# Performance work log

Hardware: AMD Instinct MI355X
Metric: run time of the kernel (lower is better)

Reference implementation:

```python
import jax, jax.numpy as jnp
import numpy as np

EMBED_DIM = 256
NUM_HEADS = 4
HEAD_DIM = EMBED_DIM // NUM_HEADS
SCALE = HEAD_DIM ** (-0.5)


def setup_inputs() -> dict:
    key = jax.random.key(0)
    kx, kq, kp, kb = jax.random.split(key, 4)
    B, N, C = 4, 4096, EMBED_DIM
    x = jax.random.normal(kx, (B, N, C), dtype=jnp.float32)
    # qkv: Linear(C, 3C, bias=False); torch stores weight as [out, in]
    w_qkv = jax.random.normal(kq, (3 * C, C), dtype=jnp.float32) * (C ** -0.5)
    w_proj = jax.random.normal(kp, (C, C), dtype=jnp.float32) * (C ** -0.5)
    b_proj = jax.random.normal(kb, (C,), dtype=jnp.float32) * 0.01
    return {"x": x, "w_qkv": w_qkv, "w_proj": w_proj, "b_proj": b_proj}


def reference(x, w_qkv, w_proj, b_proj):
    B, N, C = x.shape
    H, D = NUM_HEADS, HEAD_DIM
    # qkv projection: [B,N,3C] -> [3,B,H,N,D]
    qkv = (x @ w_qkv.T).reshape(B, N, 3, H, D).transpose(2, 0, 3, 1, 4)
    q, k, v = qkv[0], qkv[1], qkv[2]
    # materialized [B,H,N,N] scores (faithful to the original)
    attn = jnp.einsum("bhnd,bhmd->bhnm", q, k) * SCALE
    attn_probs = jax.nn.softmax(attn, axis=-1)
    out = jnp.einsum("bhnm,bhmd->bhnd", attn_probs, v)
    out = out.transpose(0, 2, 1, 3).reshape(B, N, C)
    return out @ w_proj.T + b_proj
```

## Files before the change

kernel.cpp:

```cpp
#include <hip/hip_runtime.h>
#include <hip/hip_bf16.h>

typedef __hip_bfloat16 bf16;
typedef _Float16 f16;
typedef __attribute__((ext_vector_type(8))) short bf16x8;
typedef __attribute__((ext_vector_type(8))) _Float16 f16x8;
typedef __attribute__((ext_vector_type(2))) _Float16 f16x2;
typedef __attribute__((ext_vector_type(4))) float f32x4;
typedef __attribute__((ext_vector_type(4))) unsigned int u32x4;
typedef __attribute__((ext_vector_type(2))) unsigned int u32x2;

#define B_ 4
#define N_ 4096
#define C_ 256
#define H_ 4
#define D_ 64
#define KLN 0.18033688011112042f

#if __has_builtin(__builtin_amdgcn_exp2f)
#define EXP2(x) __builtin_amdgcn_exp2f(x)
#else
#define EXP2(x) exp2f(x)
#endif
#if __has_builtin(__builtin_amdgcn_rcpf)
#define RCP(x) __builtin_amdgcn_rcpf(x)
#else
#define RCP(x) (1.0f / (x))
#endif

__device__ inline void load_lds16(const void* g, void* l) {
#if __has_builtin(__builtin_amdgcn_global_load_lds)
    __builtin_amdgcn_global_load_lds(
        (const __attribute__((address_space(1))) unsigned int*)g,
        (__attribute__((address_space(3))) unsigned int*)l, 16, 0, 0);
#else
    int ln = __lane_id();
    ((u32x4*)l)[ln] = *((const u32x4*)g);
#endif
}

__device__ inline unsigned int pk2(float a, float b) {
    unsigned int ua = __builtin_bit_cast(unsigned int, a) + 0x8000u;
    unsigned int ub = __builtin_bit_cast(unsigned int, b) + 0x8000u;
    return (ua >> 16) | (ub & 0xffff0000u);
}
__device__ inline unsigned int pkh2(float a, float b) {
#if __has_builtin(__builtin_amdgcn_cvt_pkrtz)
    return __builtin_bit_cast(unsigned int, __builtin_amdgcn_cvt_pkrtz(a, b));
#else
    f16x2 h = { (f16)a, (f16)b };
    return __builtin_bit_cast(unsigned int, h);
#endif
}
__device__ inline short f2s(float x) {
    return (short)__builtin_bit_cast(unsigned short, __float2bfloat16(x));
}
__device__ inline bf16x8 cvt8(const float* __restrict__ p) {
    f32x4 a = *reinterpret_cast<const f32x4*>(p);
    f32x4 b = *reinterpret_cast<const f32x4*>(p + 4);
    bf16x8 r = { f2s(a[0]), f2s(a[1]), f2s(a[2]), f2s(a[3]),
                 f2s(b[0]), f2s(b[1]), f2s(b[2]), f2s(b[3]) };
    return r;
}

__global__ __launch_bounds__(256) void cast_bf16(const float* __restrict__ x,
                                                 const float* __restrict__ wq,
                                                 const float* __restrict__ wp,
                                                 bf16* __restrict__ xb,
                                                 bf16* __restrict__ wqb,
                                                 bf16* __restrict__ wpb)
{
    int bid = blockIdx.x;
    const float* s; bf16* d; int base;
    if (bid < 2048)      { s = x;  d = xb;  base = bid * 2048; }
    else if (bid < 2144) { s = wq; d = wqb; base = (bid - 2048) * 2048; }
    else                 { s = wp; d = wpb; base = (bid - 2144) * 2048; }
    int i = base + threadIdx.x * 8;
    f32x4 a = *reinterpret_cast<const f32x4*>(s + i);
    f32x4 b = *reinterpret_cast<const f32x4*>(s + i + 4);
    u32x4 o;
    o.x = pk2(a[0], a[1]); o.y = pk2(a[2], a[3]);
    o.z = pk2(b[0], b[1]); o.w = pk2(b[2], b[3]);
    *reinterpret_cast<u32x4*>(d + i) = o;
}

__global__ __launch_bounds__(256, 2) void qkv_fast(const bf16* __restrict__ x,
                                                   const bf16* __restrict__ w,
                                                   bf16* __restrict__ qw,
                                                   bf16* __restrict__ kw,
                                                   f16* __restrict__ vtw)
{
    __shared__ short w_s[64][264];
    const int tid  = threadIdx.x;
    const int lane = tid & 63;
    const int wav  = tid >> 6;
    const int quad = lane >> 4;
    const int l16  = lane & 15;
    const int mt = blockIdx.x / 12, nb = blockIdx.x % 12;
    const int m0 = mt * 64, n0 = nb * 64;

    {
        const int row = tid >> 2, cb = (tid & 3) * 64;
        const bf16* src = w + (size_t)(n0 + row) * C_ + cb;
#pragma unroll
        for (int i = 0; i < 8; ++i)
            *reinterpret_cast<bf16x8*>(&w_s[row][cb + i * 8]) =
                *reinterpret_cast<const bf16x8*>(src + i * 8);
    }
    __syncthreads();

    f32x4 acc[4] = {{0,0,0,0},{0,0,0,0},{0,0,0,0},{0,0,0,0}};
    const bf16* xrow = x + (size_t)(m0 + wav * 16 + l16) * C_ + quad * 8;
#pragma unroll
    for (int k0 = 0; k0 < C_; k0 += 32) {
        bf16x8 a = *reinterpret_cast<const bf16x8*>(xrow + k0);
#pragma unroll
        for (int nt = 0; nt < 4; ++nt) {
            bf16x8 b = *reinterpret_cast<const bf16x8*>(&w_s[nt * 16 + l16][k0 + quad * 8]);
            acc[nt] = __builtin_amdgcn_mfma_f32_16x16x32_bf16(a, b, acc[nt], 0, 0, 0);
        }
    }

    const int bb = m0 >> 12;
    const int nbase = (m0 + wav * 16) & (N_ - 1);
    if (nb < 4) {
        const int h = nb;
#pragma unroll
        for (int nt = 0; nt < 4; ++nt)
#pragma unroll
            for (int r = 0; r < 4; ++r) {
                int n = nbase + quad * 4 + r, d = nt * 16 + l16;
                qw[(((size_t)bb * H_ + h) * N_ + n) * D_ + d] =
                    __float2bfloat16(acc[nt][r] * KLN);
            }
    } else if (nb < 8) {
        const int h = nb - 4;
#pragma unroll
        for (int nt = 0; nt < 4; ++nt)
#pragma unroll
            for (int r = 0; r < 4; ++r) {
                int n = nbase + quad * 4 + r, d = nt * 16 + l16;
                kw[(((size_t)bb * H_ + h) * N_ + n) * D_ + d] =
                    __float2bfloat16(acc[nt][r]);
            }
    } else {
        const int h = nb - 8;
#pragma unroll
        for (int nt = 0; nt < 4; ++nt) {
            int d = nt * 16 + l16;
            u32x2 wv;
            wv.x = pkh2(acc[nt][0], acc[nt][1]);
            wv.y = pkh2(acc[nt][2], acc[nt][3]);
            *reinterpret_cast<u32x2*>(
                vtw + (((size_t)bb * H_ + h) * D_ + d) * N_ + nbase + quad * 4) = wv;
        }
    }
}

__global__ __launch_bounds__(256) void qkv_cvt(const float* __restrict__ x,
                                               const float* __restrict__ w,
                                               bf16* __restrict__ qw,
                                               bf16* __restrict__ kw,
                                               f16* __restrict__ vtw)
{
    const int lane = threadIdx.x & 63;
    const int wav  = threadIdx.x >> 6;
    const int quad = lane >> 4;
    const int l16  = lane & 15;
    const int gw   = blockIdx.x * 4 + wav;
    const int m0   = (gw / 12) * 16;
    const int n0   = (gw % 12) * 64;

    f32x4 acc[4] = {{0,0,0,0},{0,0,0,0},{0,0,0,0},{0,0,0,0}};
    const float* xrow = x + (size_t)(m0 + l16) * C_ + quad * 8;
#pragma unroll
    for (int k0 = 0; k0 < C_; k0 += 32) {
        bf16x8 a = cvt8(xrow + k0);
#pragma unroll
        for (int nt = 0; nt < 4; ++nt) {
            bf16x8 b = cvt8(w + (size_t)(n0 + nt * 16 + l16) * C_ + k0 + quad * 8);
            acc[nt] = __builtin_amdgcn_mfma_f32_16x16x32_bf16(a, b, acc[nt], 0, 0, 0);
        }
    }
#pragma unroll
    for (int nt = 0; nt < 4; ++nt)
#pragma unroll
        for (int r = 0; r < 4; ++r) {
            int m  = m0 + quad * 4 + r;
            int o  = n0 + nt * 16 + l16;
            int bb = m >> 12;
            int n  = m & (N_ - 1);
            if (o < 256) {
                int h = o >> 6, d = o & 63;
                qw[(((size_t)bb * H_ + h) * N_ + n) * D_ + d] =
                    __float2bfloat16(acc[nt][r] * KLN);
            } else if (o < 512) {
                int oo = o - 256; int h = oo >> 6, d = oo & 63;
                kw[(((size_t)bb * H_ + h) * N_ + n) * D_ + d] =
                    __float2bfloat16(acc[nt][r]);
            } else {
                int oo = o - 512; int h = oo >> 6, d = oo & 63;
                vtw[(((size_t)bb * H_ + h) * D_ + d) * N_ + n] = (f16)acc[nt][r];
            }
        }
}

__global__ __launch_bounds__(256, 2) void attn(const bf16* __restrict__ q,
                                               const bf16* __restrict__ k,
                                               const f16* __restrict__ vt,
                                               bf16* __restrict__ o)
{
    __shared__ short        k_s[2][64 * 64];
    __shared__ f16          v_s[2][64 * 64];
    __shared__ unsigned int p_s[4][64 * 36];

    const int tid  = threadIdx.x;
    const int lane = tid & 63;
    const int wav  = tid >> 6;
    const int quad = lane >> 4;
    const int l16  = lane & 15;
    const int l8   = l16 & 7;
    const int sub  = wav & 1;
    const int jh   = wav >> 1;
    const int bh = blockIdx.x >> 5;
    const int qt = blockIdx.x & 31;
    const int bb = bh >> 2, h = bh & 3;

    const bf16* qp = q  + (size_t)bh * N_ * D_;
    const bf16* kp = k  + (size_t)bh * N_ * D_;
    const f16*  vp = vt + (size_t)bh * D_ * N_;

    const int qbase = qt * 128 + sub * 64;
    bf16x8 qb[4][2];
#pragma unroll
    for (int qg = 0; qg < 4; ++qg)
#pragma unroll
        for (int ks = 0; ks < 2; ++ks)
            qb[qg][ks] = *reinterpret_cast<const bf16x8*>(
                qp + (size_t)(qbase + qg * 16 + l16) * D_ + ks * 32 + quad * 8);

    const int ri = lane >> 3;
    const int ci = lane & 7;
    const int gc = ci ^ ri;

    f32x4 oacc[4][4];
    f32x4 lacc[4] = {{0,0,0,0},{0,0,0,0},{0,0,0,0},{0,0,0,0}};
#pragma unroll
    for (int qg = 0; qg < 4; ++qg)
#pragma unroll
        for (int dt = 0; dt < 4; ++dt) oacc[qg][dt] = (f32x4){0,0,0,0};
    const f16x8 onesA = {1.f16, 1.f16, 1.f16, 1.f16, 1.f16, 1.f16, 1.f16, 1.f16};

    for (int t = 0; t < 32; ++t) {
        const int j0 = jh * 2048 + t * 64;
        __syncthreads();
#pragma unroll
        for (int g = 0; g < 4; ++g) {
            const int rl_ = sub * 32 + g * 8;
            load_lds16(kp + (size_t)(j0 + rl_ + ri) * D_ + gc * 8, &k_s[jh][rl_ * 64]);
            load_lds16(vp + (size_t)(rl_ + ri) * N_ + j0 + gc * 8, &v_s[jh][rl_ * 64]);
        }
        __syncthreads();

        bf16x8 ka[4][2];
#pragma unroll
        for (int nt = 0; nt < 4; ++nt)
#pragma unroll
            for (int ks = 0; ks < 2; ++ks)
                ka[nt][ks] = *reinterpret_cast<const bf16x8*>(
                    &k_s[jh][(nt * 16 + l16) * 64 + (((ks << 2) + quad) ^ l8) * 8]);

#pragma unroll
        for (int qg = 0; qg < 4; ++qg) {
            f32x4 s[4] = {{0,0,0,0},{0,0,0,0},{0,0,0,0},{0,0,0,0}};
#pragma unroll
            for (int nt = 0; nt < 4; ++nt) {
                s[nt] = __builtin_amdgcn_mfma_f32_16x16x32_bf16(ka[nt][0], qb[qg][0], s[nt], 0, 0, 0);
                s[nt] = __builtin_amdgcn_mfma_f32_16x16x32_bf16(ka[nt][1], qb[qg][1], s[nt], 0, 0, 0);
            }
            unsigned int* prow = &p_s[wav][(qg * 16 + l16) * 36];
#pragma unroll
            for (int nt = 0; nt < 4; ++nt) {
                float p0 = EXP2(s[nt][0]);
                float p1 = EXP2(s[nt][1]);
                float p2 = EXP2(s[nt][2]);
                float p3 = EXP2(s[nt][3]);
                u32x2 w2 = { pkh2(p0, p1), pkh2(p2, p3) };
                *reinterpret_cast<u32x2*>(prow + nt * 8 + quad * 2) = w2;
            }
        }
        asm volatile("" ::: "memory");

#pragma unroll
        for (int ks = 0; ks < 2; ++ks) {
            f16x8 pb[4];
#pragma unroll
            for (int qg = 0; qg < 4; ++qg) {
                u32x4 pw = *reinterpret_cast<const u32x4*>(
                    &p_s[wav][(qg * 16 + l16) * 36 + ks * 16 + quad * 4]);
                pb[qg] = __builtin_bit_cast(f16x8, pw);
                lacc[qg] = __builtin_amdgcn_mfma_f32_16x16x32_f16(onesA, pb[qg], lacc[qg], 0, 0, 0);
            }
#pragma unroll
            for (int dt = 0; dt < 4; ++dt) {
                f16x8 va = *reinterpret_cast<const f16x8*>(
                    &v_s[jh][(dt * 16 + l16) * 64 + (((ks << 2) + quad) ^ l8) * 8]);
#pragma unroll
                for (int qg = 0; qg < 4; ++qg)
                    oacc[qg][dt] = __builtin_amdgcn_mfma_f32_16x16x32_f16(va, pb[qg], oacc[qg][dt], 0, 0, 0);
            }
        }
    }

    __syncthreads();
    float* mrg = reinterpret_cast<float*>(p_s);
    if (jh == 1) {
        float* dst = mrg + (sub * 64 + lane) * 68;
#pragma unroll
        for (int qg = 0; qg < 4; ++qg) {
#pragma unroll
            for (int dt = 0; dt < 4; ++dt)
#pragma unroll
                for (int e = 0; e < 4; ++e)
                    dst[qg * 17 + dt * 4 + e] = oacc[qg][dt][e];
            dst[qg * 17 + 16] = lacc[qg][0];
        }
    }
    __syncthreads();
    if (jh == 0) {
        const float* src = mrg + (sub * 64 + lane) * 68;
#pragma unroll
        for (int qg = 0; qg < 4; ++qg) {
            float rl = RCP(lacc[qg][0] + src[qg * 17 + 16]);
            const size_t obase = ((size_t)bb * N_ + qbase + qg * 16 + l16) * C_ + h * D_;
#pragma unroll
            for (int dt = 0; dt < 4; ++dt) {
                float v0 = (oacc[qg][dt][0] + src[qg * 17 + dt * 4 + 0]) * rl;
                float v1 = (oacc[qg][dt][1] + src[qg * 17 + dt * 4 + 1]) * rl;
                float v2 = (oacc[qg][dt][2] + src[qg * 17 + dt * 4 + 2]) * rl;
                float v3 = (oacc[qg][dt][3] + src[qg * 17 + dt * 4 + 3]) * rl;
                u32x2 wv = { pk2(v0, v1), pk2(v2, v3) };
                *reinterpret_cast<u32x2*>(o + obase + dt * 16 + quad * 4) = wv;
            }
        }
    }
}

__global__ __launch_bounds__(256, 2) void out_proj_fast(const bf16* __restrict__ ov,
                                                        const bf16* __restrict__ w,
                                                        const float* __restrict__ bias,
                                                        float* __restrict__ out)
{
    __shared__ short w_s[64][264];
    const int tid  = threadIdx.x;
    const int lane = tid & 63;
    const int wav  = tid >> 6;
    const int quad = lane >> 4;
    const int l16  = lane & 15;
    const int m0 = (blockIdx.x >> 2) * 64;
    const int n0 = (blockIdx.x & 3) * 64;

    {
        const int row = tid >> 2, cb = (tid & 3) * 64;
        const bf16* src = w + (size_t)(n0 + row) * C_ + cb;
#pragma unroll
        for (int i = 0; i < 8; ++i)
            *reinterpret_cast<bf16x8*>(&w_s[row][cb + i * 8]) =
                *reinterpret_cast<const bf16x8*>(src + i * 8);
    }
    __syncthreads();

    f32x4 acc[4] = {{0,0,0,0},{0,0,0,0},{0,0,0,0},{0,0,0,0}};
    const bf16* orow = ov + (size_t)(m0 + wav * 16 + l16) * C_ + quad * 8;
#pragma unroll
    for (int k0 = 0; k0 < C_; k0 += 32) {
        bf16x8 a = *reinterpret_cast<const bf16x8*>(orow + k0);
#pragma unroll
        for (int nt = 0; nt < 4; ++nt) {
            bf16x8 b = *reinterpret_cast<const bf16x8*>(&w_s[nt * 16 + l16][k0 + quad * 8]);
            acc[nt] = __builtin_amdgcn_mfma_f32_16x16x32_bf16(a, b, acc[nt], 0, 0, 0);
        }
    }
#pragma unroll
    for (int nt = 0; nt < 4; ++nt)
#pragma unroll
        for (int r = 0; r < 4; ++r) {
            int m  = m0 + wav * 16 + quad * 4 + r;
            int oc = n0 + nt * 16 + l16;
            out[(size_t)m * C_ + oc] = acc[nt][r] + bias[oc];
        }
}

__global__ __launch_bounds__(256) void out_proj_cvt(const bf16* __restrict__ ov,
                                                    const float* __restrict__ w,
                                                    const float* __restrict__ bias,
                                                    float* __restrict__ out)
{
    const int lane = threadIdx.x & 63;
    const int wav  = threadIdx.x >> 6;
    const int quad = lane >> 4;
    const int l16  = lane & 15;
    const int gw   = blockIdx.x * 4 + wav;
    const int m0   = (gw >> 2) * 16;
    const int n0   = (gw & 3) * 64;

    f32x4 acc[4] = {{0,0,0,0},{0,0,0,0},{0,0,0,0},{0,0,0,0}};
    const bf16* orow = ov + (size_t)(m0 + l16) * C_ + quad * 8;
#pragma unroll
    for (int k0 = 0; k0 < C_; k0 += 32) {
        bf16x8 a = *reinterpret_cast<const bf16x8*>(orow + k0);
#pragma unroll
        for (int nt = 0; nt < 4; ++nt) {
            bf16x8 b = cvt8(w + (size_t)(n0 + nt * 16 + l16) * C_ + k0 + quad * 8);
            acc[nt] = __builtin_amdgcn_mfma_f32_16x16x32_bf16(a, b, acc[nt], 0, 0, 0);
        }
    }
#pragma unroll
    for (int nt = 0; nt < 4; ++nt)
#pragma unroll
        for (int r = 0; r < 4; ++r) {
            int m  = m0 + quad * 4 + r;
            int oc = n0 + nt * 16 + l16;
            out[(size_t)m * C_ + oc] = acc[nt][r] + bias[oc];
        }
}

extern "C" void kernel_launch(void* const* d_in, const int* in_sizes, int n_in,
                              void* d_out, int out_size, void* d_ws, size_t ws_size,
                              hipStream_t stream) {
    const float* x      = (const float*)d_in[0];
    const float* w_qkv  = (const float*)d_in[1];
    const float* w_proj = (const float*)d_in[2];
    const float* b_proj = (const float*)d_in[3];
    float* out = (float*)d_out;

    const size_t qkv_elems = (size_t)B_ * H_ * N_ * D_;
    bf16* q_ws  = (bf16*)d_ws;
    bf16* k_ws  = q_ws  + qkv_elems;
    f16*  vt_ws = (f16*)(k_ws + qkv_elems);
    bf16* o_ws  = (bf16*)(vt_ws + qkv_elems);
    bf16* x_bf  = o_ws  + qkv_elems;
    bf16* wq_bf = x_bf  + (size_t)B_ * N_ * C_;
    bf16* wp_bf = wq_bf + (size_t)3 * C_ * C_;

    const size_t need = ((size_t)4 * qkv_elems + (size_t)B_ * N_ * C_
                         + (size_t)3 * C_ * C_ + (size_t)C_ * C_) * 2;

    if (ws_size >= need) {
        cast_bf16    <<<2176, 256, 0, stream>>>(x, w_qkv, w_proj, x_bf, wq_bf, wp_bf);
        qkv_fast     <<<3072, 256, 0, stream>>>(x_bf, wq_bf, q_ws, k_ws, vt_ws);
        attn         <<< 512, 256, 0, stream>>>(q_ws, k_ws, vt_ws, o_ws);
        out_proj_fast<<<1024, 256, 0, stream>>>(o_ws, wp_bf, b_proj, out);
    } else {
        qkv_cvt      <<<3072, 256, 0, stream>>>(x, w_qkv, q_ws, k_ws, vt_ws);
        attn         <<< 512, 256, 0, stream>>>(q_ws, k_ws, vt_ws, o_ws);
        out_proj_cvt <<<1024, 256, 0, stream>>>(o_ws, w_proj, b_proj, out);
    }
}
```

Baseline: 186.5 us.

## Fuse casts into projections and prepack K/V for LDS-free attention

Removes the separate bf16 cast kernel and converts fp32 x and weights inside the QKV and output projection kernels. The QKV kernel now writes K and V^T in a fragment-packed layout so the attention kernel loads MFMA operands straight from global memory into registers, with K double-buffered across tiles, instead of staging K/V through LDS behind barriers. The row-sum is now accumulated with scalar adds and cross-lane shuffles rather than an extra MFMA against a ones vector, and block indexing is remapped for locality. In exchange, attention depends on direct global loads with no LDS reuse across waves, which raises global and L2 traffic and register pressure.

Result: slower. 301.4 us (+61.6%).

```diff
diff --git a/kernel.cpp b/kernel.cpp
--- a/kernel.cpp
+++ b/kernel.cpp
@@ -28,17 +28,6 @@
 #define RCP(x) (1.0f / (x))
 #endif
 
-__device__ inline void load_lds16(const void* g, void* l) {
-#if __has_builtin(__builtin_amdgcn_global_load_lds)
-    __builtin_amdgcn_global_load_lds(
-        (const __attribute__((address_space(1))) unsigned int*)g,
-        (__attribute__((address_space(3))) unsigned int*)l, 16, 0, 0);
-#else
-    int ln = __lane_id();
-    ((u32x4*)l)[ln] = *((const u32x4*)g);
-#endif
-}
-
 __device__ inline unsigned int pk2(float a, float b) {
     unsigned int ua = __builtin_bit_cast(unsigned int, a) + 0x8000u;
     unsigned int ub = __builtin_bit_cast(unsigned int, b) + 0x8000u;
@@ -52,43 +41,18 @@
     return __builtin_bit_cast(unsigned int, h);
 #endif
 }
-__device__ inline short f2s(float x) {
-    return (short)__builtin_bit_cast(unsigned short, __float2bfloat16(x));
-}
 __device__ inline bf16x8 cvt8(const float* __restrict__ p) {
     f32x4 a = *reinterpret_cast<const f32x4*>(p);
     f32x4 b = *reinterpret_cast<const f32x4*>(p + 4);
-    bf16x8 r = { f2s(a[0]), f2s(a[1]), f2s(a[2]), f2s(a[3]),
-                 f2s(b[0]), f2s(b[1]), f2s(b[2]), f2s(b[3]) };
-    return r;
-}
-
-__global__ __launch_bounds__(256) void cast_bf16(const float* __restrict__ x,
-                                                 const float* __restrict__ wq,
-                                                 const float* __restrict__ wp,
-                                                 bf16* __restrict__ xb,
-                                                 bf16* __restrict__ wqb,
-                                                 bf16* __restrict__ wpb)
-{
-    int bid = blockIdx.x;
-    const float* s; bf16* d; int base;
-    if (bid < 2048)      { s = x;  d = xb;  base = bid * 2048; }
-    else if (bid < 2144) { s = wq; d = wqb; base = (bid - 2048) * 2048; }
-    else                 { s = wp; d = wpb; base = (bid - 2144) * 2048; }
-    int i = base + threadIdx.x * 8;
-    f32x4 a = *reinterpret_cast<const f32x4*>(s + i);
-    f32x4 b = *reinterpret_cast<const f32x4*>(s + i + 4);
-    u32x4 o;
-    o.x = pk2(a[0], a[1]); o.y = pk2(a[2], a[3]);
-    o.z = pk2(b[0], b[1]); o.w = pk2(b[2], b[3]);
-    *reinterpret_cast<u32x4*>(d + i) = o;
-}
-
-__global__ __launch_bounds__(256, 2) void qkv_fast(const bf16* __restrict__ x,
-                                                   const bf16* __restrict__ w,
-                                                   bf16* __restrict__ qw,
-                                                   bf16* __restrict__ kw,
-                                                   f16* __restrict__ vtw)
+    u32x4 r = { pk2(a[0], a[1]), pk2(a[2], a[3]), pk2(b[0], b[1]), pk2(b[2], b[3]) };
+    return __builtin_bit_cast(bf16x8, r);
+}
+
+__global__ __launch_bounds__(256, 2) void qkv_fused(const float* __restrict__ x,
+                                                    const float* __restrict__ w,
+                                                    bf16* __restrict__ qw,
+                                                    bf16* __restrict__ kw,
+                                                    f16* __restrict__ vtw)
 {
     __shared__ short w_s[64][264];
     const int tid  = threadIdx.x;
@@ -96,24 +60,28 @@
     const int wav  = tid >> 6;
     const int quad = lane >> 4;
     const int l16  = lane & 15;
-    const int mt = blockIdx.x / 12, nb = blockIdx.x % 12;
+    const int mt = blockIdx.x & 255, nb = blockIdx.x >> 8;
     const int m0 = mt * 64, n0 = nb * 64;
 
     {
         const int row = tid >> 2, cb = (tid & 3) * 64;
-        const bf16* src = w + (size_t)(n0 + row) * C_ + cb;
-#pragma unroll
-        for (int i = 0; i < 8; ++i)
-            *reinterpret_cast<bf16x8*>(&w_s[row][cb + i * 8]) =
-                *reinterpret_cast<const bf16x8*>(src + i * 8);
+        const float* src = w + (size_t)(n0 + row) * C_ + cb;
+#pragma unroll
+        for (int i = 0; i < 8; ++i) {
+            f32x4 a = *reinterpret_cast<const f32x4*>(src + i * 8);
+            f32x4 b = *reinterpret_cast<const f32x4*>(src + i * 8 + 4);
+            u32x4 pkd = { pk2(a[0], a[1]), pk2(a[2], a[3]),
+                          pk2(b[0], b[1]), pk2(b[2], b[3]) };
+            *reinterpret_cast<u32x4*>(&w_s[row][cb + i * 8]) = pkd;
+        }
     }
     __syncthreads();
 
     f32x4 acc[4] = {{0,0,0,0},{0,0,0,0},{0,0,0,0},{0,0,0,0}};
-    const bf16* xrow = x + (size_t)(m0 + wav * 16 + l16) * C_ + quad * 8;
+    const float* xrow = x + (size_t)(m0 + wav * 16 + l16) * C_ + quad * 8;
 #pragma unroll
     for (int k0 = 0; k0 < C_; k0 += 32) {
-        bf16x8 a = *reinterpret_cast<const bf16x8*>(xrow + k0);
+        bf16x8 a = cvt8(xrow + k0);
 #pragma unroll
         for (int nt = 0; nt < 4; ++nt) {
             bf16x8 b = *reinterpret_cast<const bf16x8*>(&w_s[nt * 16 + l16][k0 + quad * 8]);
@@ -135,83 +103,37 @@
             }
     } else if (nb < 8) {
         const int h = nb - 4;
-#pragma unroll
-        for (int nt = 0; nt < 4; ++nt)
-#pragma unroll
-            for (int r = 0; r < 4; ++r) {
-                int n = nbase + quad * 4 + r, d = nt * 16 + l16;
-                kw[(((size_t)bb * H_ + h) * N_ + n) * D_ + d] =
-                    __float2bfloat16(acc[nt][r]);
-            }
+        bf16* kb_ = kw + (size_t)(bb * H_ + h) * (N_ / 16) * 1024;
+        const int jblk = nbase >> 4;
+#pragma unroll
+        for (int nt = 0; nt < 4; ++nt) {
+            const int base = jblk * 1024 + (nt >> 1) * 512 +
+                             (((nt * 2) + (l16 >> 3)) & 3) * 128 + (l16 & 7);
+#pragma unroll
+            for (int r = 0; r < 4; ++r)
+                kb_[base + (quad * 4 + r) * 8] = __float2bfloat16(acc[nt][r]);
+        }
     } else {
         const int h = nb - 8;
+        f16* vb_ = vtw + (size_t)(bb * H_ + h) * (N_ / 64) * 4096;
+        const int jblk64 = nbase >> 6;
+        const int ksv    = (nbase >> 5) & 1;
+        const int quadv  = (((nbase & 31) + quad * 4) >> 3) & 3;
+        const int ev     = (quad & 1) * 4;
 #pragma unroll
         for (int nt = 0; nt < 4; ++nt) {
-            int d = nt * 16 + l16;
-            u32x2 wv;
-            wv.x = pkh2(acc[nt][0], acc[nt][1]);
-            wv.y = pkh2(acc[nt][2], acc[nt][3]);
+            u32x2 wv = { pkh2(acc[nt][0], acc[nt][1]), pkh2(acc[nt][2], acc[nt][3]) };
             *reinterpret_cast<u32x2*>(
-                vtw + (((size_t)bb * H_ + h) * D_ + d) * N_ + nbase + quad * 4) = wv;
-        }
-    }
-}
-
-__global__ __launch_bounds__(256) void qkv_cvt(const float* __restrict__ x,
-                                               const float* __restrict__ w,
-                                               bf16* __restrict__ qw,
-                                               bf16* __restrict__ kw,
-                                               f16* __restrict__ vtw)
-{
-    const int lane = threadIdx.x & 63;
-    const int wav  = threadIdx.x >> 6;
-    const int quad = lane >> 4;
-    const int l16  = lane & 15;
-    const int gw   = blockIdx.x * 4 + wav;
-    const int m0   = (gw / 12) * 16;
-    const int n0   = (gw % 12) * 64;
-
-    f32x4 acc[4] = {{0,0,0,0},{0,0,0,0},{0,0,0,0},{0,0,0,0}};
-    const float* xrow = x + (size_t)(m0 + l16) * C_ + quad * 8;
-#pragma unroll
-    for (int k0 = 0; k0 < C_; k0 += 32) {
-        bf16x8 a = cvt8(xrow + k0);
-#pragma unroll
-        for (int nt = 0; nt < 4; ++nt) {
-            bf16x8 b = cvt8(w + (size_t)(n0 + nt * 16 + l16) * C_ + k0 + quad * 8);
-            acc[nt] = __builtin_amdgcn_mfma_f32_16x16x32_bf16(a, b, acc[nt], 0, 0, 0);
-        }
-    }
-#pragma unroll
-    for (int nt = 0; nt < 4; ++nt)
-#pragma unroll
-        for (int r = 0; r < 4; ++r) {
-            int m  = m0 + quad * 4 + r;
-            int o  = n0 + nt * 16 + l16;
-            int bb = m >> 12;
-            int n  = m & (N_ - 1);
-            if (o < 256) {
-                int h = o >> 6, d = o & 63;
-                qw[(((size_t)bb * H_ + h) * N_ + n) * D_ + d] =
-                    __float2bfloat16(acc[nt][r] * KLN);
-            } else if (o < 512) {
-                int oo = o - 256; int h = oo >> 6, d = oo & 63;
-                kw[(((size_t)bb * H_ + h) * N_ + n) * D_ + d] =
-                    __float2bfloat16(acc[nt][r]);
-            } else {
-                int oo = o - 512; int h = oo >> 6, d = oo & 63;
-                vtw[(((size_t)bb * H_ + h) * D_ + d) * N_ + n] = (f16)acc[nt][r];
-            }
-        }
+                &vb_[jblk64 * 4096 + nt * 1024 + ksv * 512 + (quadv * 16 + l16) * 8 + ev]) = wv;
+        }
+    }
 }
 
 __global__ __launch_bounds__(256, 2) void attn(const bf16* __restrict__ q,
-                                               const bf16* __restrict__ k,
+                                               const bf16* __restrict__ kt,
                                                const f16* __restrict__ vt,
                                                bf16* __restrict__ o)
 {
-    __shared__ short        k_s[2][64 * 64];
-    __shared__ f16          v_s[2][64 * 64];
     __shared__ unsigned int p_s[4][64 * 36];
 
     const int tid  = threadIdx.x;
@@ -219,16 +141,15 @@
     const int wav  = tid >> 6;
     const int quad = lane >> 4;
     const int l16  = lane & 15;
-    const int l8   = l16 & 7;
     const int sub  = wav & 1;
     const int jh   = wav >> 1;
-    const int bh = blockIdx.x >> 5;
-    const int qt = blockIdx.x & 31;
+    const int bh = (blockIdx.x & 7) | (((blockIdx.x >> 3) & 1) << 3);
+    const int qt = blockIdx.x >> 4;
     const int bb = bh >> 2, h = bh & 3;
 
-    const bf16* qp = q  + (size_t)bh * N_ * D_;
-    const bf16* kp = k  + (size_t)bh * N_ * D_;
-    const f16*  vp = vt + (size_t)bh * D_ * N_;
+    const bf16* qp  = q  + (size_t)bh * N_ * D_;
+    const bf16* ktp = kt + (size_t)bh * (N_ / 16) * 1024 + lane * 8;
+    const f16*  vtp = vt + (size_t)bh * (N_ / 64) * 4096 + lane * 8;
 
     const int qbase = qt * 128 + sub * 64;
     bf16x8 qb[4][2];
@@ -239,55 +160,62 @@
             qb[qg][ks] = *reinterpret_cast<const bf16x8*>(
                 qp + (size_t)(qbase + qg * 16 + l16) * D_ + ks * 32 + quad * 8);
 
-    const int ri = lane >> 3;
-    const int ci = lane & 7;
-    const int gc = ci ^ ri;
-
     f32x4 oacc[4][4];
-    f32x4 lacc[4] = {{0,0,0,0},{0,0,0,0},{0,0,0,0},{0,0,0,0}};
 #pragma unroll
     for (int qg = 0; qg < 4; ++qg)
 #pragma unroll
         for (int dt = 0; dt < 4; ++dt) oacc[qg][dt] = (f32x4){0,0,0,0};
-    const f16x8 onesA = {1.f16, 1.f16, 1.f16, 1.f16, 1.f16, 1.f16, 1.f16, 1.f16};
-
-    for (int t = 0; t < 32; ++t) {
-        const int j0 = jh * 2048 + t * 64;
-        __syncthreads();
-#pragma unroll
-        for (int g = 0; g < 4; ++g) {
-            const int rl_ = sub * 32 + g * 8;
-            load_lds16(kp + (size_t)(j0 + rl_ + ri) * D_ + gc * 8, &k_s[jh][rl_ * 64]);
-            load_lds16(vp + (size_t)(rl_ + ri) * N_ + j0 + gc * 8, &v_s[jh][rl_ * 64]);
-        }
-        __syncthreads();
-
-        bf16x8 ka[4][2];
+    float lsum[4] = {0.f, 0.f, 0.f, 0.f};
+
+    bf16x8 kA[4][2], kB[4][2];
+    {
+        const int jb0 = (jh * 2048) >> 4;
 #pragma unroll
         for (int nt = 0; nt < 4; ++nt)
 #pragma unroll
             for (int ks = 0; ks < 2; ++ks)
-                ka[nt][ks] = *reinterpret_cast<const bf16x8*>(
-                    &k_s[jh][(nt * 16 + l16) * 64 + (((ks << 2) + quad) ^ l8) * 8]);
-
+                kA[nt][ks] = *reinterpret_cast<const bf16x8*>(
+                    ktp + (size_t)(jb0 + nt) * 1024 + ks * 512);
+    }
+
+    auto tile = [&](bf16x8 (&kc)[4][2], bf16x8 (&kn)[4][2], int t) {
+        f16x8 va[2][4];
+#pragma unroll
+        for (int ks = 0; ks < 2; ++ks)
+#pragma unroll
+            for (int dt = 0; dt < 4; ++dt)
+                va[ks][dt] = *reinterpret_cast<const f16x8*>(
+                    vtp + (size_t)(jh * 32 + t) * 4096 + dt * 1024 + ks * 512);
+        if (t < 31) {
+            const int jbn = ((jh * 2048 + (t + 1) * 64) >> 4);
+#pragma unroll
+            for (int nt = 0; nt < 4; ++nt)
+#pragma unroll
+                for (int ks = 0; ks < 2; ++ks)
+                    kn[nt][ks] = *reinterpret_cast<const bf16x8*>(
+                        ktp + (size_t)(jbn + nt) * 1024 + ks * 512);
+        }
 #pragma unroll
         for (int qg = 0; qg < 4; ++qg) {
             f32x4 s[4] = {{0,0,0,0},{0,0,0,0},{0,0,0,0},{0,0,0,0}};
 #pragma unroll
             for (int nt = 0; nt < 4; ++nt) {
-                s[nt] = __builtin_amdgcn_mfma_f32_16x16x32_bf16(ka[nt][0], qb[qg][0], s[nt], 0, 0, 0);
-                s[nt] = __builtin_amdgcn_mfma_f32_16x16x32_bf16(ka[nt][1], qb[qg][1], s[nt], 0, 0, 0);
+                s[nt] = __builtin_amdgcn_mfma_f32_16x16x32_bf16(kc[nt][0], qb[qg][0], s[nt], 0, 0, 0);
+                s[nt] = __builtin_amdgcn_mfma_f32_16x16x32_bf16(kc[nt][1], qb[qg][1], s[nt], 0, 0, 0);
             }
             unsigned int* prow = &p_s[wav][(qg * 16 + l16) * 36];
+            float lq = 0.f;
 #pragma unroll
             for (int nt = 0; nt < 4; ++nt) {
                 float p0 = EXP2(s[nt][0]);
                 float p1 = EXP2(s[nt][1]);
                 float p2 = EXP2(s[nt][2]);
                 float p3 = EXP2(s[nt][3]);
+                lq += (p0 + p1) + (p2 + p3);
                 u32x2 w2 = { pkh2(p0, p1), pkh2(p2, p3) };
                 *reinterpret_cast<u32x2*>(prow + nt * 8 + quad * 2) = w2;
             }
+            lsum[qg] += lq;
         }
         asm volatile("" ::: "memory");
 
@@ -299,17 +227,24 @@
                 u32x4 pw = *reinterpret_cast<const u32x4*>(
                     &p_s[wav][(qg * 16 + l16) * 36 + ks * 16 + quad * 4]);
                 pb[qg] = __builtin_bit_cast(f16x8, pw);
-                lacc[qg] = __builtin_amdgcn_mfma_f32_16x16x32_f16(onesA, pb[qg], lacc[qg], 0, 0, 0);
-            }
-#pragma unroll
-            for (int dt = 0; dt < 4; ++dt) {
-                f16x8 va = *reinterpret_cast<const f16x8*>(
-                    &v_s[jh][(dt * 16 + l16) * 64 + (((ks << 2) + quad) ^ l8) * 8]);
+            }
+#pragma unroll
+            for (int dt = 0; dt < 4; ++dt)
 #pragma unroll
                 for (int qg = 0; qg < 4; ++qg)
-                    oacc[qg][dt] = __builtin_amdgcn_mfma_f32_16x16x32_f16(va, pb[qg], oacc[qg][dt], 0, 0, 0);
-            }
-        }
+                    oacc[qg][dt] = __builtin_amdgcn_mfma_f32_16x16x32_f16(va[ks][dt], pb[qg], oacc[qg][dt], 0, 0, 0);
+        }
+    };
+
+    for (int t = 0; t < 32; t += 2) {
+        tile(kA, kB, t);
+        tile(kB, kA, t + 1);
+    }
+
+#pragma unroll
+    for (int qg = 0; qg < 4; ++qg) {
+        lsum[qg] += __shfl_xor(lsum[qg], 16, 64);
+        lsum[qg] += __shfl_xor(lsum[qg], 32, 64);
     }
 
     __syncthreads();
@@ -323,7 +258,7 @@
 #pragma unroll
                 for (int e = 0; e < 4; ++e)
                     dst[qg * 17 + dt * 4 + e] = oacc[qg][dt][e];
-            dst[qg * 17 + 16] = lacc[qg][0];
+            dst[qg * 17 + 16] = lsum[qg];
         }
     }
     __syncthreads();
@@ -331,7 +266,7 @@
         const float* src = mrg + (sub * 64 + lane) * 68;
 #pragma unroll
         for (int qg = 0; qg < 4; ++qg) {
-            float rl = RCP(lacc[qg][0] + src[qg * 17 + 16]);
+            float rl = RCP(lsum[qg] + src[qg * 17 + 16]);
             const size_t obase = ((size_t)bb * N_ + qbase + qg * 16 + l16) * C_ + h * D_;
 #pragma unroll
             for (int dt = 0; dt < 4; ++dt) {
@@ -346,10 +281,10 @@
     }
 }
 
-__global__ __launch_bounds__(256, 2) void out_proj_fast(const bf16* __restrict__ ov,
-                                                        const bf16* __restrict__ w,
-                                                        const float* __restrict__ bias,
-                                                        float* __restrict__ out)
+__global__ __launch_bounds__(256, 2) void out_proj(const bf16* __restrict__ ov,
+                                                   const float* __restrict__ w,
+                                                   const float* __restrict__ bias,
+                                                   float* __restrict__ out)
 {
     __shared__ short w_s[64][264];
     const int tid  = threadIdx.x;
@@ -362,11 +297,15 @@
 
     {
         const int row = tid >> 2, cb = (tid & 3) * 64;
-        const bf16* src = w + (size_t)(n0 + row) * C_ + cb;
-#pragma unroll
-        for (int i = 0; i < 8; ++i)
-            *reinterpret_cast<bf16x8*>(&w_s[row][cb + i * 8]) =
-                *reinterpret_cast<const bf16x8*>(src + i * 8);
+        const float* src = w + (size_t)(n0 + row) * C_ + cb;
+#pragma unroll
+        for (int i = 0; i < 8; ++i) {
+            f32x4 a = *reinterpret_cast<const f32x4*>(src + i * 8);
+            f32x4 b = *reinterpret_cast<const f32x4*>(src + i * 8 + 4);
+            u32x4 pkd = { pk2(a[0], a[1]), pk2(a[2], a[3]),
+                          pk2(b[0], b[1]), pk2(b[2], b[3]) };
+            *reinterpret_cast<u32x4*>(&w_s[row][cb + i * 8]) = pkd;
+        }
     }
     __syncthreads();
 
@@ -386,40 +325,6 @@
 #pragma unroll
         for (int r = 0; r < 4; ++r) {
             int m  = m0 + wav * 16 + quad * 4 + r;
-            int oc = n0 + nt * 16 + l16;
-            out[(size_t)m * C_ + oc] = acc[nt][r] + bias[oc];
-        }
-}
-
-__global__ __launch_bounds__(256) void out_proj_cvt(const bf16* __restrict__ ov,
-                                                    const float* __restrict__ w,
-                                                    const float* __restrict__ bias,
-                                                    float* __restrict__ out)
-{
-    const int lane = threadIdx.x & 63;
-    const int wav  = threadIdx.x >> 6;
-    const int quad = lane >> 4;
-    const int l16  = lane & 15;
-    const int gw   = blockIdx.x * 4 + wav;
-    const int m0   = (gw >> 2) * 16;
-    const int n0   = (gw & 3) * 64;
-
-    f32x4 acc[4] = {{0,0,0,0},{0,0,0,0},{0,0,0,0},{0,0,0,0}};
-    const bf16* orow = ov + (size_t)(m0 + l16) * C_ + quad * 8;
-#pragma unroll
-    for (int k0 = 0; k0 < C_; k0 += 32) {
-        bf16x8 a = *reinterpret_cast<const bf16x8*>(orow + k0);
-#pragma unroll
-        for (int nt = 0; nt < 4; ++nt) {
-            bf16x8 b = cvt8(w + (size_t)(n0 + nt * 16 + l16) * C_ + k0 + quad * 8);
-            acc[nt] = __builtin_amdgcn_mfma_f32_16x16x32_bf16(a, b, acc[nt], 0, 0, 0);
-        }
-    }
-#pragma unroll
-    for (int nt = 0; nt < 4; ++nt)
-#pragma unroll
-        for (int r = 0; r < 4; ++r) {
-            int m  = m0 + quad * 4 + r;
             int oc = n0 + nt * 16 + l16;
             out[(size_t)m * C_ + oc] = acc[nt][r] + bias[oc];
         }
@@ -436,24 +341,11 @@
 
     const size_t qkv_elems = (size_t)B_ * H_ * N_ * D_;
     bf16* q_ws  = (bf16*)d_ws;
-    bf16* k_ws  = q_ws  + qkv_elems;
+    bf16* k_ws  = q_ws + qkv_elems;
     f16*  vt_ws = (f16*)(k_ws + qkv_elems);
     bf16* o_ws  = (bf16*)(vt_ws + qkv_elems);
-    bf16* x_bf  = o_ws  + qkv_elems;
-    bf16* wq_bf = x_bf  + (size_t)B_ * N_ * C_;
-    bf16* wp_bf = wq_bf + (size_t)3 * C_ * C_;
-
-    const size_t need = ((size_t)4 * qkv_elems + (size_t)B_ * N_ * C_
-                         + (size_t)3 * C_ * C_ + (size_t)C_ * C_) * 2;
-
-    if (ws_size >= need) {
-        cast_bf16    <<<2176, 256, 0, stream>>>(x, w_qkv, w_proj, x_bf, wq_bf, wp_bf);
-        qkv_fast     <<<3072, 256, 0, stream>>>(x_bf, wq_bf, q_ws, k_ws, vt_ws);
-        attn         <<< 512, 256, 0, stream>>>(q_ws, k_ws, vt_ws, o_ws);
-        out_proj_fast<<<1024, 256, 0, stream>>>(o_ws, wp_bf, b_proj, out);
-    } else {
-        qkv_cvt      <<<3072, 256, 0, stream>>>(x, w_qkv, q_ws, k_ws, vt_ws);
-        attn         <<< 512, 256, 0, stream>>>(q_ws, k_ws, vt_ws, o_ws);
-        out_proj_cvt <<<1024, 256, 0, stream>>>(o_ws, w_proj, b_proj, out);
-    }
-}
+
+    qkv_fused<<<3072, 256, 0, stream>>>(x, w_qkv, q_ws, k_ws, vt_ws);
+    attn     <<< 512, 256, 0, stream>>>(q_ws, k_ws, vt_ws, o_ws);
+    out_proj <<<1024, 256, 0, stream>>>(o_ws, w_proj, b_proj, out);
+}
```
